# Performance work log

Measured on AMD Instinct MI355X. Metric: run time of the kernel, lower is better.

## Reference

```python
import jax, jax.numpy as jnp
import numpy as np

NEG = -1e10
EPS = 1e-5
H = 4  # num_heads


def layer_norm(y, g, b):
    m = jnp.mean(y, axis=-1, keepdims=True)
    v = jnp.mean((y - m) ** 2, axis=-1, keepdims=True)
    return (y - m) * jax.lax.rsqrt(v + EPS) * g + b


def setup_inputs() -> dict:
    key = jax.random.key(0)
    B, N, C = 16, 1024, 256
    ks = jax.random.split(key, 12)
    std = 0.1  # matches trunc_normal_(std=0.1) init
    inp = {
        "x": jax.random.normal(ks[0], (B, N, C), jnp.float32),
        "K": jax.random.normal(ks[1], (B, N, N), jnp.float32),
        "n1": jax.random.randint(ks[2], (B,), 8, 33),
        "n2": jax.random.randint(ks[3], (B,), 8, 33),
        "qkv_w": jax.random.normal(ks[4], (3 * C, C), jnp.float32) * std,
        "qkv_b": jnp.zeros((3 * C,), jnp.float32),
        "proj_w": jax.random.normal(ks[5], (C, C), jnp.float32) * std,
        "proj_b": jnp.zeros((C,), jnp.float32),
        "ln1_g": jnp.ones((C,), jnp.float32),
        "ln1_b": jnp.zeros((C,), jnp.float32),
        "ln2_g": jnp.ones((C,), jnp.float32),
        "ln2_b": jnp.zeros((C,), jnp.float32),
        "fc1_w": jax.random.normal(ks[6], (4 * C, C), jnp.float32) * std,
        "fc1_b": jnp.zeros((4 * C,), jnp.float32),
        "fc2_w": jax.random.normal(ks[7], (C, 4 * C), jnp.float32) * std,
        "fc2_b": jnp.zeros((C,), jnp.float32),
    }
    return inp


def reference(x, K, n1, n2, qkv_w, qkv_b, proj_w, proj_b,
              ln1_g, ln1_b, ln2_g, ln2_b, fc1_w, fc1_b, fc2_w, fc2_b):
    B, N, C = x.shape
    D = C // H
    scale = D ** -0.5

    # --- attention block ---
    h = layer_norm(x, ln1_g, ln1_b)
    qkv = (h @ qkv_w.T + qkv_b).reshape(B, N, 3, H, D)
    qkv = jnp.transpose(qkv, (2, 0, 3, 1, 4))  # [3,B,H,N,D]
    q, k, v = qkv[0], qkv[1], qkv[2]

    attn = jnp.einsum('bhnd,bhmd->bhnm', q, k) * scale  # [B,H,N,N]

    # per-sample dynamic block mask: rows>=n1*n2 fully masked; cols>=n1*n2 masked
    nrc = (n1 * n2)[:, None]                  # [B,1]
    invalid = jnp.arange(N)[None, :] >= nrc   # [B,N]
    mask = invalid[:, :, None] | invalid[:, None, :]  # [B,N,N]
    attn = jnp.where(mask[:, None], NEG, attn)
    attn = attn + K[:, None]                  # broadcast K over heads

    a = jax.nn.softmax(attn, axis=-1)
    o = jnp.einsum('bhnm,bhmd->bhnd', a, v)
    o = jnp.transpose(o, (0, 2, 1, 3)).reshape(B, N, C)
    x = x + (o @ proj_w.T + proj_b)

    # --- MLP block (exact GELU as torch nn.GELU) ---
    h2 = layer_norm(x, ln2_g, ln2_b)
    m = jax.nn.gelu(h2 @ fc1_w.T + fc1_b, approximate=False)
    m = m @ fc2_w.T + fc2_b
    return x + m
```

## Files before the change

kernel.cpp:

```cpp
#include <hip/hip_runtime.h>
#include <math.h>
#include <stdint.h>

constexpr int Bc = 16, Nn = 1024, Cc = 256, Hh = 4;
constexpr int Mrows = Bc * Nn;
constexpr float EPSV = 1e-5f;

typedef __attribute__((ext_vector_type(4))) float f32x4;
typedef __attribute__((ext_vector_type(8))) short bf16x8;

__device__ inline float wave_reduce_sum(float v) {
#pragma unroll
  for (int m = 32; m >= 1; m >>= 1) v += __shfl_xor(v, m);
  return v;
}

__device__ inline short f2bf(float f) {
  uint32_t u = __builtin_bit_cast(uint32_t, f);
  u = (u + 0x7fffu + ((u >> 16) & 1u)) >> 16;
  return (short)u;
}
__device__ inline float bf2f(short s) {
  uint32_t u = ((uint32_t)(uint16_t)s) << 16;
  return __builtin_bit_cast(float, u);
}

__device__ inline float gelu_fast(float x) {
  float x2 = x * x;
  float u = x * (0.7978845608028654f + 0.0356774081f * x2);
  float e = __builtin_amdgcn_exp2f(u * 2.8853900817779268f);
  return x * (1.f - __builtin_amdgcn_rcpf(e + 1.f));
}

#define GLDS(gptr, lptr)                                             \
  __builtin_amdgcn_global_load_lds(                                  \
      (const __attribute__((address_space(1))) void*)(gptr),         \
      (__attribute__((address_space(3))) void*)(lptr), 16, 0, 0)

__global__ __launch_bounds__(256)
void cvt_all(const float* __restrict__ s0, short* __restrict__ d0,
             const float* __restrict__ s1, short* __restrict__ d1,
             const float* __restrict__ s2, short* __restrict__ d2,
             const float* __restrict__ s3, short* __restrict__ d3) {
  int bid = blockIdx.x;
  const float* s;
  short* d;
  int base;
  if (bid < 192)      { s = s0; d = d0; base = bid; }
  else if (bid < 256) { s = s1; d = d1; base = bid - 192; }
  else if (bid < 512) { s = s2; d = d2; base = bid - 256; }
  else                { s = s3; d = d3; base = bid - 512; }
  int i = (base * 256 + threadIdx.x) * 4;
  float4 v = *(const float4*)(s + i);
  short4 o;
  o.x = f2bf(v.x); o.y = f2bf(v.y); o.z = f2bf(v.z); o.w = f2bf(v.w);
  *(short4*)(d + i) = o;
}

__global__ __launch_bounds__(256)
void ln_kernel(const float* __restrict__ x, const float* __restrict__ g,
               const float* __restrict__ b, short* __restrict__ h) {
  int row = blockIdx.x * 4 + (threadIdx.x >> 6);
  int lane = threadIdx.x & 63;
  const float4* xr = (const float4*)(x + (size_t)row * Cc);
  float4 v = xr[lane];
  float s = v.x + v.y + v.z + v.w;
  float sq = v.x * v.x + v.y * v.y + v.z * v.z + v.w * v.w;
  s = wave_reduce_sum(s);
  sq = wave_reduce_sum(sq);
  float mean = s * (1.f / Cc);
  float var = sq * (1.f / Cc) - mean * mean;
  float inv = rsqrtf(var + EPSV);
  float4 gg = ((const float4*)g)[lane];
  float4 bb = ((const float4*)b)[lane];
  short4 o;
  o.x = f2bf((v.x - mean) * inv * gg.x + bb.x);
  o.y = f2bf((v.y - mean) * inv * gg.y + bb.y);
  o.z = f2bf((v.z - mean) * inv * gg.z + bb.z);
  o.w = f2bf((v.w - mean) * inv * gg.w + bb.w);
  *(short4*)(h + (size_t)row * Cc + lane * 4) = o;
}

__global__ __launch_bounds__(256)
void qkv_mfma(const short* __restrict__ A, const short* __restrict__ Bw,
              const float* __restrict__ bias, short* __restrict__ qkp,
              short* __restrict__ vtp) {
  __shared__ __align__(16) short As[128 * 64];
  __shared__ __align__(16) short Bs[128 * 64];
  int t = threadIdx.x;
  int w = t >> 6, lane = t & 63;
  int wm = w >> 1, wn = w & 1;
  int l16 = lane & 15, lhi = lane >> 4;
  int m0 = blockIdx.y * 128, n0 = blockIdx.x * 128;
  const bool vblk = (n0 >= 512);
  f32x4 acc[4][4] = {};

  for (int k0 = 0; k0 < 256; k0 += 64) {
    __syncthreads();
#pragma unroll
    for (int i = 0; i < 4; ++i) {
      int cc = i * 256 + t;
      int r = cc >> 3, sl = cc & 7, ssl = sl ^ (r & 7);
      GLDS(A + (size_t)(m0 + r) * 256 + k0 + ssl * 8, &As[cc * 8]);
      GLDS(Bw + (size_t)(n0 + r) * 256 + k0 + ssl * 8, &Bs[cc * 8]);
    }
    asm volatile("s_waitcnt vmcnt(0)" ::: "memory");
    __syncthreads();
    if (!vblk) {
#pragma unroll
      for (int ks = 0; ks < 2; ++ks) {
        bf16x8 af[4], bg[4];
#pragma unroll
        for (int mi = 0; mi < 4; ++mi) {
          int row = wm * 64 + mi * 16 + l16;
          af[mi] = *(const bf16x8*)&As[row * 64 + ((ks * 32 + lhi * 8) ^ ((row & 7) << 3))];
        }
#pragma unroll
        for (int ni = 0; ni < 4; ++ni) {
          int row = wn * 64 + ni * 16 + l16;
          bg[ni] = *(const bf16x8*)&Bs[row * 64 + ((ks * 32 + lhi * 8) ^ ((row & 7) << 3))];
        }
#pragma unroll
        for (int mi = 0; mi < 4; ++mi)
#pragma unroll
          for (int ni = 0; ni < 4; ++ni)
            acc[mi][ni] = __builtin_amdgcn_mfma_f32_16x16x32_bf16(
                af[mi], bg[ni], acc[mi][ni], 0, 0, 0);
      }
    } else {
#pragma unroll
      for (int ks = 0; ks < 2; ++ks) {
        bf16x8 af[4], bg[4];
#pragma unroll
        for (int mi = 0; mi < 4; ++mi) {
          int row = wm * 64 + mi * 16 + l16;
          af[mi] = *(const bf16x8*)&As[row * 64 + ((ks * 32 + lhi * 8) ^ ((row & 7) << 3))];
        }
#pragma unroll
        for (int ni = 0; ni < 4; ++ni) {
          int row = wn * 64 + ni * 16 + l16;
          bg[ni] = *(const bf16x8*)&Bs[row * 64 + ((ks * 32 + lhi * 8) ^ ((row & 7) << 3))];
        }
#pragma unroll
        for (int mi = 0; mi < 4; ++mi)
#pragma unroll
          for (int ni = 0; ni < 4; ++ni)
            acc[mi][ni] = __builtin_amdgcn_mfma_f32_16x16x32_bf16(
                bg[ni], af[mi], acc[mi][ni], 0, 0, 0);
      }
    }
  }

  if (!vblk) {
    const bool isq = (n0 < 256);
#pragma unroll
    for (int mi = 0; mi < 4; ++mi) {
      int mbase = m0 + wm * 64 + mi * 16 + lhi * 4;
#pragma unroll
      for (int ni = 0; ni < 4; ++ni) {
        int n = n0 + wn * 64 + ni * 16 + l16;
        int s = n >> 8, hh = (n >> 6) & 3, d = n & 63;
        float bv = bias[n];
#pragma unroll
        for (int r = 0; r < 4; ++r) {
          int m = mbase + r;
          int b = m >> 10, rw = m & 1023;
          float v = acc[mi][ni][r] + bv;
          if (isq) v *= 0.125f;
          qkp[(size_t)s * 4194304 + (((size_t)(b * 4 + hh)) * 1024 + rw) * 64 + d] = f2bf(v);
        }
      }
    }
  } else {
#pragma unroll
    for (int mi = 0; mi < 4; ++mi) {
#pragma unroll
      for (int ni = 0; ni < 4; ++ni) {
#pragma unroll
        for (int r = 0; r < 4; ++r) {
          int n = n0 + wn * 64 + ni * 16 + lhi * 4 + r;
          int hh = (n >> 6) & 3, d = n & 63;
          int m = m0 + wm * 64 + mi * 16 + l16;
          int b = m >> 10, rw = m & 1023;
          float v = acc[mi][ni][r] + bias[n];
          vtp[(((size_t)(b * 4 + hh)) * 64 + d) * 1024 + rw] = f2bf(v);
        }
      }
    }
  }
}

__global__ __launch_bounds__(256)
void vmean_kernel(const short* __restrict__ vt, short* __restrict__ vmb) {
  __shared__ float part[64][4];
  int bh = blockIdx.x;
  int d = threadIdx.x >> 2, seg = threadIdx.x & 3;
  const short* p = vt + (size_t)bh * 65536 + (size_t)d * 1024 + seg * 256;
  float s = 0.f;
  for (int i = 0; i < 256; i += 8) {
    bf16x8 v = *(const bf16x8*)(p + i);
#pragma unroll
    for (int j = 0; j < 8; ++j) s += bf2f(v[j]);
  }
  part[d][seg] = s;
  __syncthreads();
  if (threadIdx.x < 64) {
    int dd = threadIdx.x;
    float tot = part[dd][0] + part[dd][1] + part[dd][2] + part[dd][3];
    vmb[bh * 64 + dd] = f2bf(tot * (1.f / 1024.f));
  }
}

__global__ __launch_bounds__(256)
void fattn_mfma(const short* __restrict__ qpk, const short* __restrict__ kpk,
                const short* __restrict__ vt, const float* __restrict__ Kmat,
                const int* __restrict__ n1, const int* __restrict__ n2,
                const short* __restrict__ vmb, short* __restrict__ o,
                float* __restrict__ pO, float* __restrict__ pL, int zsplit) {
  int bh = blockIdx.y, b = bh >> 2, hh = bh & 3;
  int qt = blockIdx.x;
  int row0 = qt * 64;
  int sp = blockIdx.z;
  int t = threadIdx.x;
  int w = t >> 6, lane = t & 63, l16 = lane & 15, lhi = lane >> 4;

  const short* qb = qpk + (size_t)bh * 65536 + (size_t)(row0 + w * 16 + l16) * 64;
  bf16x8 qf0 = *(const bf16x8*)(qb + lhi * 8);
  bf16x8 qf1 = *(const bf16x8*)(qb + 32 + lhi * 8);

  int nc = n1[b] * n2[b];
  __shared__ short vms[64];
  if (t < 64) vms[t] = vmb[bh * 64 + t];
  __syncthreads();
  if (row0 >= nc) {
    if (sp == 0) {
      for (int idx = t; idx < 4096; idx += 256) {
        int r = idx >> 6, d = idx & 63;
        o[((size_t)(b * 1024 + row0 + r)) * 256 + hh * 64 + d] = vms[d];
      }
    }
    return;
  }
  int ntiles = (nc + 63) >> 6;
  int TPS = (zsplit == 1) ? ntiles : ((ntiles + 3) >> 2);
  int nsp = (ntiles + TPS - 1) / TPS;
  int jt0 = sp * TPS;
  if (jt0 >= ntiles) return;
  int jstart = jt0 * 64;
  int jend = min(jstart + TPS * 64, nc);
  const bool final_out = (nsp == 1);

  __shared__ __align__(16) short Ks[2][64 * 64];
  __shared__ __align__(16) short Vs[2][64 * 64];
  __shared__ __align__(16) short Ps[64 * 64];

  constexpr float LOG2E = 1.4426950408889634f;
  constexpr float MREF = 12.0f;

  f32x4 accO[4] = {};
  float lsum[4] = {};
  const float* Kb = Kmat + (size_t)b * 1048576 + (size_t)(row0 + w * 16) * 1024;

  f32x4 kvp[4];

#pragma unroll
  for (int i = 0; i < 2; ++i) {
    int cc = i * 256 + t;
    int r = cc >> 3, sl = cc & 7, ssl = sl ^ (r & 7);
    GLDS(kpk + (size_t)bh * 65536 + (size_t)(jstart + r) * 64 + ssl * 8, &Ks[0][cc * 8]);
    GLDS(vt + (size_t)bh * 65536 + (size_t)r * 1024 + jstart + ssl * 8, &Vs[0][cc * 8]);
  }
#pragma unroll
  for (int ni = 0; ni < 4; ++ni)
#pragma unroll
    for (int r = 0; r < 4; ++r)
      kvp[ni][r] =
          (Kb[(size_t)(lhi * 4 + r) * 1024 + jstart + ni * 16 + l16] - MREF) * LOG2E;

  int cur = 0;
  for (int j0 = jstart; j0 < jend; j0 += 64, cur ^= 1) {
    asm volatile("s_waitcnt vmcnt(0)" ::: "memory");
    __syncthreads();

    f32x4 kvc[4];
#pragma unroll
    for (int i = 0; i < 4; ++i) kvc[i] = kvp[i];
    int jn = j0 + 64;
    if (jn < jend) {
      int nxt = cur ^ 1;
#pragma unroll
      for (int i = 0; i < 2; ++i) {
        int cc = i * 256 + t;
        int r = cc >> 3, sl = cc & 7, ssl = sl ^ (r & 7);
        GLDS(kpk + (size_t)bh * 65536 + (size_t)(jn + r) * 64 + ssl * 8, &Ks[nxt][cc * 8]);
        GLDS(vt + (size_t)bh * 65536 + (size_t)r * 1024 + jn + ssl * 8, &Vs[nxt][cc * 8]);
      }
#pragma unroll
      for (int ni = 0; ni < 4; ++ni)
#pragma unroll
        for (int r = 0; r < 4; ++r)
          kvp[ni][r] =
              (Kb[(size_t)(lhi * 4 + r) * 1024 + jn + ni * 16 + l16] - MREF) * LOG2E;
    }

    f32x4 accS[4] = {};
#pragma unroll
    for (int ks = 0; ks < 2; ++ks) {
#pragma unroll
      for (int ni = 0; ni < 4; ++ni) {
        int row = ni * 16 + l16;
        bf16x8 kf = *(const bf16x8*)&Ks[cur][row * 64 + (((ks * 4 + lhi) ^ (row & 7)) << 3)];
        accS[ni] = __builtin_amdgcn_mfma_f32_16x16x32_bf16(
            ks ? qf1 : qf0, kf, accS[ni], 0, 0, 0);
      }
    }

#pragma unroll
    for (int ni = 0; ni < 4; ++ni) {
      bool valid = (j0 + ni * 16 + l16) < nc;
#pragma unroll
      for (int r = 0; r < 4; ++r) {
        float e = __builtin_amdgcn_exp2f(fmaf(accS[ni][r], LOG2E, kvc[ni][r]));
        e = valid ? e : 0.f;
        lsum[r] += e;
        int prow = w * 16 + lhi * 4 + r;
        int col = ni * 16 + l16;
        Ps[prow * 64 + ((((col >> 3) ^ (prow & 7)) << 3) | (col & 7))] = f2bf(e);
      }
    }

#pragma unroll
    for (int ks = 0; ks < 2; ++ks) {
      int prow = w * 16 + l16;
      bf16x8 pf = *(const bf16x8*)&Ps[prow * 64 + (((ks * 4 + lhi) ^ (prow & 7)) << 3)];
#pragma unroll
      for (int ni = 0; ni < 4; ++ni) {
        int vrow = ni * 16 + l16;
        bf16x8 vf = *(const bf16x8*)&Vs[cur][vrow * 64 + (((ks * 4 + lhi) ^ (vrow & 7)) << 3)];
        accO[ni] = __builtin_amdgcn_mfma_f32_16x16x32_bf16(pf, vf, accO[ni], 0, 0, 0);
      }
    }
  }

#pragma unroll
  for (int r = 0; r < 4; ++r) {
    lsum[r] += __shfl_xor(lsum[r], 1);
    lsum[r] += __shfl_xor(lsum[r], 2);
    lsum[r] += __shfl_xor(lsum[r], 4);
    lsum[r] += __shfl_xor(lsum[r], 8);
  }

  if (final_out) {
#pragma unroll
    for (int ni = 0; ni < 4; ++ni) {
#pragma unroll
      for (int r = 0; r < 4; ++r) {
        int row = row0 + w * 16 + lhi * 4 + r;
        int d = ni * 16 + l16;
        short ov;
        if (row < nc) ov = f2bf(accO[ni][r] * (1.f / lsum[r]));
        else ov = vms[d];
        o[((size_t)(b * 1024 + row)) * 256 + hh * 64 + d] = ov;
      }
    }
  } else {
    float* po = pO + (((size_t)sp * 64 + bh) * 16 + qt) * 4096;
#pragma unroll
    for (int ni = 0; ni < 4; ++ni)
#pragma unroll
      for (int r = 0; r < 4; ++r)
        po[(w * 16 + lhi * 4 + r) * 64 + ni * 16 + l16] = accO[ni][r];
    if (l16 == 0) {
      float* pl = pL + (((size_t)sp * 64 + bh) * 16 + qt) * 64;
#pragma unroll
      for (int r = 0; r < 4; ++r) pl[w * 16 + lhi * 4 + r] = lsum[r];
    }
    if (sp == 0) {
      for (int idx = t; idx < 4096; idx += 256) {
        int r = idx >> 6, d = idx & 63;
        int row = row0 + r;
        if (row >= nc)
          o[((size_t)(b * 1024 + row)) * 256 + hh * 64 + d] = vms[d];
      }
    }
  }
}

__global__ __launch_bounds__(256)
void fattn_combine(const float* __restrict__ pO, const float* __restrict__ pL,
                   const int* __restrict__ n1, const int* __restrict__ n2,
                   short* __restrict__ o) {
  int bh = blockIdx.y, b = bh >> 2, hh = bh & 3;
  int qt = blockIdx.x;
  int row0 = qt * 64;
  int nc = n1[b] * n2[b];
  if (row0 >= nc) return;
  int ntiles = (nc + 63) >> 6;
  int TPS = (ntiles + 3) >> 2;
  int nsp = (ntiles + TPS - 1) / TPS;
  if (nsp < 2) return;

  int t = threadIdx.x;
  int q = t >> 2, ds = (t & 3) * 16;
  int row = row0 + q;
  if (row >= nc) return;

  const size_t spstrideO = (size_t)64 * 16 * 4096;
  const size_t spstrideL = (size_t)64 * 16 * 64;
  const float* baseO = pO + ((size_t)bh * 16 + qt) * 4096 + q * 64 + ds;
  const float* baseL = pL + ((size_t)bh * 16 + qt) * 64 + q;

  f32x4 s[4] = {};
  float L = 0.f;
  for (int sp = 0; sp < nsp; ++sp) {
    const float* p = baseO + sp * spstrideO;
#pragma unroll
    for (int i = 0; i < 4; ++i) s[i] += *(const f32x4*)(p + i * 4);
    L += baseL[sp * spstrideL];
  }
  float rl = 1.f / L;
  short* op = o + ((size_t)(b * 1024 + row)) * 256 + hh * 64 + ds;
#pragma unroll
  for (int i = 0; i < 4; ++i) {
    short4 ov;
    ov.x = f2bf(s[i][0] * rl);
    ov.y = f2bf(s[i][1] * rl);
    ov.z = f2bf(s[i][2] * rl);
    ov.w = f2bf(s[i][3] * rl);
    *(short4*)(op + i * 4) = ov;
  }
}

template <bool GELU, bool RES, bool OUTF, bool OUTB>
__global__ __launch_bounds__(256)
void gemm_mfma(const short* __restrict__ A, const short* __restrict__ Bw,
               const float* __restrict__ bias, const float* __restrict__ resid,
               float* __restrict__ Cf, short* __restrict__ Cb,
               int M, int Nd, int Kd) {
  __shared__ __align__(16) short As[128 * 64];
  __shared__ __align__(16) short Bs[128 * 64];
  int t = threadIdx.x;
  int w = t >> 6, lane = t & 63;
  int wm = w >> 1, wn = w & 1;
  int l16 = lane & 15, lhi = lane >> 4;
  int m0 = blockIdx.y * 128, n0 = blockIdx.x * 128;
  f32x4 acc[4][4] = {};

  for (int k0 = 0; k0 < Kd; k0 += 64) {
    __syncthreads();
#pragma unroll
    for (int i = 0; i < 4; ++i) {
      int cc = i * 256 + t;
      int r = cc >> 3, sl = cc & 7, ssl = sl ^ (r & 7);
      GLDS(A + (size_t)(m0 + r) * Kd + k0 + ssl * 8, &As[cc * 8]);
      GLDS(Bw + (size_t)(n0 + r) * Kd + k0 + ssl * 8, &Bs[cc * 8]);
    }
    asm volatile("s_waitcnt vmcnt(0)" ::: "memory");
    __syncthreads();
#pragma unroll
    for (int ks = 0; ks < 2; ++ks) {
      bf16x8 af[4], bg[4];
#pragma unroll
      for (int mi = 0; mi < 4; ++mi) {
        int row = wm * 64 + mi * 16 + l16;
        af[mi] = *(const bf16x8*)&As[row * 64 + ((ks * 32 + lhi * 8) ^ ((row & 7) << 3))];
      }
#pragma unroll
      for (int ni = 0; ni < 4; ++ni) {
        int row = wn * 64 + ni * 16 + l16;
        bg[ni] = *(const bf16x8*)&Bs[row * 64 + ((ks * 32 + lhi * 8) ^ ((row & 7) << 3))];
      }
#pragma unroll
      for (int mi = 0; mi < 4; ++mi)
#pragma unroll
        for (int ni = 0; ni < 4; ++ni)
          acc[mi][ni] = __builtin_amdgcn_mfma_f32_16x16x32_bf16(
              af[mi], bg[ni], acc[mi][ni], 0, 0, 0);
    }
  }
#pragma unroll
  for (int mi = 0; mi < 4; ++mi) {
    int rbase = m0 + wm * 64 + mi * 16 + lhi * 4;
#pragma unroll
    for (int ni = 0; ni < 4; ++ni) {
      int n = n0 + wn * 64 + ni * 16 + l16;
      float bv = bias[n];
#pragma unroll
      for (int r = 0; r < 4; ++r) {
        int m = rbase + r;
        float v = acc[mi][ni][r] + bv;
        if (GELU) v = gelu_fast(v);
        size_t idx = (size_t)m * Nd + n;
        if (RES) v += resid[idx];
        if (OUTF) Cf[idx] = v;
        if (OUTB) Cb[idx] = f2bf(v);
      }
    }
  }
}

template <bool GELU, bool RES, bool OUTF, bool OUTB>
__global__ __launch_bounds__(256)
void gemm64_mfma(const short* __restrict__ A, const short* __restrict__ Bw,
                 const float* __restrict__ bias, const float* __restrict__ resid,
                 float* __restrict__ Cf, short* __restrict__ Cb,
                 int M, int Nd, int Kd) {
  __shared__ __align__(16) short As[64 * 64];
  __shared__ __align__(16) short Bs[128 * 64];
  int t = threadIdx.x;
  int w = t >> 6, lane = t & 63;
  int l16 = lane & 15, lhi = lane >> 4;
  int m0 = blockIdx.y * 64, n0 = blockIdx.x * 128;
  f32x4 acc[4][2] = {};

  for (int k0 = 0; k0 < Kd; k0 += 64) {
    __syncthreads();
#pragma unroll
    for (int i = 0; i < 2; ++i) {
      int cc = i * 256 + t;
      int r = cc >> 3, sl = cc & 7, ssl = sl ^ (r & 7);
      GLDS(A + (size_t)(m0 + r) * Kd + k0 + ssl * 8, &As[cc * 8]);
    }
#pragma unroll
    for (int i = 0; i < 4; ++i) {
      int cc = i * 256 + t;
      int r = cc >> 3, sl = cc & 7, ssl = sl ^ (r & 7);
      GLDS(Bw + (size_t)(n0 + r) * Kd + k0 + ssl * 8, &Bs[cc * 8]);
    }
    asm volatile("s_waitcnt vmcnt(0)" ::: "memory");
    __syncthreads();
#pragma unroll
    for (int ks = 0; ks < 2; ++ks) {
      bf16x8 af[4], bg[2];
#pragma unroll
      for (int mi = 0; mi < 4; ++mi) {
        int row = mi * 16 + l16;
        af[mi] = *(const bf16x8*)&As[row * 64 + ((ks * 32 + lhi * 8) ^ ((row & 7) << 3))];
      }
#pragma unroll
      for (int ni = 0; ni < 2; ++ni) {
        int row = w * 32 + ni * 16 + l16;
        bg[ni] = *(const bf16x8*)&Bs[row * 64 + ((ks * 32 + lhi * 8) ^ ((row & 7) << 3))];
      }
#pragma unroll
      for (int mi = 0; mi < 4; ++mi)
#pragma unroll
        for (int ni = 0; ni < 2; ++ni)
          acc[mi][ni] = __builtin_amdgcn_mfma_f32_16x16x32_bf16(
              af[mi], bg[ni], acc[mi][ni], 0, 0, 0);
    }
  }
#pragma unroll
  for (int mi = 0; mi < 4; ++mi) {
    int rbase = m0 + mi * 16 + lhi * 4;
#pragma unroll
    for (int ni = 0; ni < 2; ++ni) {
      int n = n0 + w * 32 + ni * 16 + l16;
      float bv = bias[n];
#pragma unroll
      for (int r = 0; r < 4; ++r) {
        int m = rbase + r;
        float v = acc[mi][ni][r] + bv;
        if (GELU) v = gelu_fast(v);
        size_t idx = (size_t)m * Nd + n;
        if (RES) v += resid[idx];
        if (OUTF) Cf[idx] = v;
        if (OUTB) Cb[idx] = f2bf(v);
      }
    }
  }
}

extern "C" void kernel_launch(void* const* d_in, const int* in_sizes, int n_in,
                              void* d_out, int out_size, void* d_ws, size_t ws_size,
                              hipStream_t stream) {
  const float* x      = (const float*)d_in[0];
  const float* Kmat   = (const float*)d_in[1];
  const int*   n1     = (const int*)d_in[2];
  const int*   n2     = (const int*)d_in[3];
  const float* qkv_w  = (const float*)d_in[4];
  const float* qkv_b  = (const float*)d_in[5];
  const float* proj_w = (const float*)d_in[6];
  const float* proj_b = (const float*)d_in[7];
  const float* ln1_g  = (const float*)d_in[8];
  const float* ln1_b  = (const float*)d_in[9];
  const float* ln2_g  = (const float*)d_in[10];
  const float* ln2_b  = (const float*)d_in[11];
  const float* fc1_w  = (const float*)d_in[12];
  const float* fc1_b  = (const float*)d_in[13];
  const float* fc2_w  = (const float*)d_in[14];
  const float* fc2_b  = (const float*)d_in[15];
  float* out = (float*)d_out;

  char* ws = (char*)d_ws;
  constexpr size_t MB = 1024 * 1024;
  short* hb    = (short*)ws;
  short* qkp   = (short*)(ws + 8 * MB);
  short* vtp   = (short*)(ws + 24 * MB);
  short* m1    = (short*)(ws + 8 * MB);
  short* vmb   = (short*)(ws + 40 * MB);
  short* wqkv  = (short*)(ws + 41 * MB);
  short* wproj = (short*)(ws + 42 * MB);
  short* wfc1  = (short*)(ws + 43 * MB);
  short* wfc2  = (short*)(ws + 44 * MB);
  float* pO    = (float*)(ws + 48 * MB);
  float* pL    = (float*)(ws + 116 * MB);
  short* obuf  = hb;
  short* qpk   = qkp;
  short* kpk   = qkp + 4194304;

  const bool split = ws_size >= (size_t)118 * MB;

  cvt_all<<<dim3(768), 256, 0, stream>>>(qkv_w, wqkv, proj_w, wproj,
                                         fc1_w, wfc1, fc2_w, wfc2);
  ln_kernel<<<dim3(Mrows / 4), 256, 0, stream>>>(x, ln1_g, ln1_b, hb);
  qkv_mfma<<<dim3(6, 128), 256, 0, stream>>>(hb, wqkv, qkv_b, qkp, vtp);
  vmean_kernel<<<dim3(Bc * Hh), 256, 0, stream>>>(vtp, vmb);
  if (split) {
    fattn_mfma<<<dim3(Nn / 64, Bc * Hh, 4), 256, 0, stream>>>(
        qpk, kpk, vtp, Kmat, n1, n2, vmb, obuf, pO, pL, 4);
    fattn_combine<<<dim3(Nn / 64, Bc * Hh), 256, 0, stream>>>(
        pO, pL, n1, n2, obuf);
  } else {
    fattn_mfma<<<dim3(Nn / 64, Bc * Hh, 1), 256, 0, stream>>>(
        qpk, kpk, vtp, Kmat, n1, n2, vmb, obuf, pO, pL, 1);
  }
  gemm64_mfma<false, true, true, false><<<dim3(2, 256), 256, 0, stream>>>(
      obuf, wproj, proj_b, x, out, nullptr, Mrows, 256, 256);
  ln_kernel<<<dim3(Mrows / 4), 256, 0, stream>>>(out, ln2_g, ln2_b, hb);
  gemm_mfma<true, false, false, true><<<dim3(8, 128), 256, 0, stream>>>(
      hb, wfc1, fc1_b, nullptr, nullptr, m1, Mrows, 1024, 256);
  gemm64_mfma<false, true, true, false><<<dim3(2, 256), 256, 0, stream>>>(
      m1, wfc2, fc2_b, out, out, nullptr, Mrows, 256, 1024);
}
```

Before: 141.9 us.

## Replace attention grid with persistent work-queue kernel sorted by sequence length

Builds a per-call work queue of (batch, head, query-tile, split) items ordered by descending valid length. A fixed set of persistent blocks then pulls items atomically instead of launching a full grid where many blocks exit early. The masked-row mean fill moves into a separate small kernel. This aims to cut wasted block launches and tail imbalance across batches, at the cost of two extra launches, a serial single-thread queue build and a per-item atomic.

```diff
diff --git a/kernel.cpp b/kernel.cpp
--- a/kernel.cpp
+++ b/kernel.cpp
@@ -212,175 +212,228 @@
 }
 
 __global__ __launch_bounds__(256)
-void fattn_mfma(const short* __restrict__ qpk, const short* __restrict__ kpk,
+void build_queue(const int* __restrict__ n1, const int* __restrict__ n2,
+                 int* __restrict__ q) {
+  __shared__ int ncs[16], order[16], boff[17];
+  int t = threadIdx.x;
+  if (t < 16) ncs[t] = n1[t] * n2[t];
+  __syncthreads();
+  if (t == 0) {
+    for (int i = 0; i < 16; ++i) order[i] = i;
+    for (int i = 1; i < 16; ++i) {
+      int oi = order[i], key = ncs[oi], j = i - 1;
+      while (j >= 0 && ncs[order[j]] < key) { order[j + 1] = order[j]; --j; }
+      order[j + 1] = oi;
+    }
+    int off = 0;
+    for (int i = 0; i < 16; ++i) {
+      boff[i] = off;
+      int nc = ncs[order[i]];
+      int nt = (nc + 63) >> 6;
+      int tps = (nt + 3) >> 2;
+      int nsp = (nt + tps - 1) / tps;
+      off += 4 * nt * nsp;
+    }
+    boff[16] = off;
+    q[0] = 0;
+    q[1] = off;
+  }
+  __syncthreads();
+  int M = boff[16];
+  for (int idx = t; idx < M; idx += 256) {
+    int s = 0;
+    while (boff[s + 1] <= idx) ++s;
+    int loc = idx - boff[s];
+    int b = order[s];
+    int nc = ncs[b];
+    int nt = (nc + 63) >> 6;
+    int tps = (nt + 3) >> 2;
+    int nsp = (nt + tps - 1) / tps;
+    int sp = loc % nsp;
+    int hq = loc / nsp;
+    int qt = hq % nt;
+    int h = hq / nt;
+    q[2 + idx] = ((b * 4 + h) << 6) | (qt << 2) | sp;
+  }
+}
+
+__global__ __launch_bounds__(256)
+void fill_mean(const int* __restrict__ n1, const int* __restrict__ n2,
+               const short* __restrict__ vmb, short* __restrict__ o) {
+  int bh = blockIdx.x, b = bh >> 2, hh = bh & 3;
+  int nc = n1[b] * n2[b];
+  int row0 = ((nc + 63) >> 6) * 64;
+  int t = threadIdx.x;
+  short vm = vmb[bh * 64 + (t & 63)];
+  for (int r = row0 + (t >> 6); r < 1024; r += 4)
+    o[((size_t)(b * 1024 + r)) * 256 + hh * 64 + (t & 63)] = vm;
+}
+
+__global__ __launch_bounds__(256)
+void fattn_pers(const short* __restrict__ qpk, const short* __restrict__ kpk,
                 const short* __restrict__ vt, const float* __restrict__ Kmat,
                 const int* __restrict__ n1, const int* __restrict__ n2,
                 const short* __restrict__ vmb, short* __restrict__ o,
-                float* __restrict__ pO, float* __restrict__ pL, int zsplit) {
-  int bh = blockIdx.y, b = bh >> 2, hh = bh & 3;
-  int qt = blockIdx.x;
-  int row0 = qt * 64;
-  int sp = blockIdx.z;
-  int t = threadIdx.x;
-  int w = t >> 6, lane = t & 63, l16 = lane & 15, lhi = lane >> 4;
-
-  const short* qb = qpk + (size_t)bh * 65536 + (size_t)(row0 + w * 16 + l16) * 64;
-  bf16x8 qf0 = *(const bf16x8*)(qb + lhi * 8);
-  bf16x8 qf1 = *(const bf16x8*)(qb + 32 + lhi * 8);
-
-  int nc = n1[b] * n2[b];
-  __shared__ short vms[64];
-  if (t < 64) vms[t] = vmb[bh * 64 + t];
-  __syncthreads();
-  if (row0 >= nc) {
-    if (sp == 0) {
-      for (int idx = t; idx < 4096; idx += 256) {
-        int r = idx >> 6, d = idx & 63;
-        o[((size_t)(b * 1024 + row0 + r)) * 256 + hh * 64 + d] = vms[d];
-      }
-    }
-    return;
-  }
-  int ntiles = (nc + 63) >> 6;
-  int TPS = (zsplit == 1) ? ntiles : ((ntiles + 3) >> 2);
-  int nsp = (ntiles + TPS - 1) / TPS;
-  int jt0 = sp * TPS;
-  if (jt0 >= ntiles) return;
-  int jstart = jt0 * 64;
-  int jend = min(jstart + TPS * 64, nc);
-  const bool final_out = (nsp == 1);
-
+                float* __restrict__ pO, float* __restrict__ pL,
+                int* __restrict__ q) {
+  __shared__ int sitem;
   __shared__ __align__(16) short Ks[2][64 * 64];
   __shared__ __align__(16) short Vs[2][64 * 64];
   __shared__ __align__(16) short Ps[64 * 64];
+  int t = threadIdx.x;
+  int w = t >> 6, lane = t & 63, l16 = lane & 15, lhi = lane >> 4;
+  const int M = q[1];
 
   constexpr float LOG2E = 1.4426950408889634f;
   constexpr float MREF = 12.0f;
 
-  f32x4 accO[4] = {};
-  float lsum[4] = {};
-  const float* Kb = Kmat + (size_t)b * 1048576 + (size_t)(row0 + w * 16) * 1024;
-
-  f32x4 kvp[4];
-
-#pragma unroll
-  for (int i = 0; i < 2; ++i) {
-    int cc = i * 256 + t;
-    int r = cc >> 3, sl = cc & 7, ssl = sl ^ (r & 7);
-    GLDS(kpk + (size_t)bh * 65536 + (size_t)(jstart + r) * 64 + ssl * 8, &Ks[0][cc * 8]);
-    GLDS(vt + (size_t)bh * 65536 + (size_t)r * 1024 + jstart + ssl * 8, &Vs[0][cc * 8]);
-  }
-#pragma unroll
-  for (int ni = 0; ni < 4; ++ni)
-#pragma unroll
-    for (int r = 0; r < 4; ++r)
-      kvp[ni][r] =
-          (Kb[(size_t)(lhi * 4 + r) * 1024 + jstart + ni * 16 + l16] - MREF) * LOG2E;
-
-  int cur = 0;
-  for (int j0 = jstart; j0 < jend; j0 += 64, cur ^= 1) {
-    asm volatile("s_waitcnt vmcnt(0)" ::: "memory");
-    __syncthreads();
-
-    f32x4 kvc[4];
-#pragma unroll
-    for (int i = 0; i < 4; ++i) kvc[i] = kvp[i];
-    int jn = j0 + 64;
-    if (jn < jend) {
-      int nxt = cur ^ 1;
-#pragma unroll
-      for (int i = 0; i < 2; ++i) {
-        int cc = i * 256 + t;
-        int r = cc >> 3, sl = cc & 7, ssl = sl ^ (r & 7);
-        GLDS(kpk + (size_t)bh * 65536 + (size_t)(jn + r) * 64 + ssl * 8, &Ks[nxt][cc * 8]);
-        GLDS(vt + (size_t)bh * 65536 + (size_t)r * 1024 + jn + ssl * 8, &Vs[nxt][cc * 8]);
-      }
+  while (true) {
+    __syncthreads();
+    if (t == 0) sitem = atomicAdd(q, 1);
+    __syncthreads();
+    int ii = sitem;
+    if (ii >= M) break;
+    int item = q[2 + ii];
+    int sp = item & 3, qt = (item >> 2) & 15, bh = item >> 6;
+    int b = bh >> 2, hh = bh & 3;
+    int row0 = qt * 64;
+    int nc = n1[b] * n2[b];
+    int ntiles = (nc + 63) >> 6;
+    int TPS = (ntiles + 3) >> 2;
+    int nsp = (ntiles + TPS - 1) / TPS;
+    int jstart = sp * TPS * 64;
+    int jend = min(jstart + TPS * 64, nc);
+    const bool final_out = (nsp == 1);
+
+    const short* qb = qpk + (size_t)bh * 65536 + (size_t)(row0 + w * 16 + l16) * 64;
+    bf16x8 qf0 = *(const bf16x8*)(qb + lhi * 8);
+    bf16x8 qf1 = *(const bf16x8*)(qb + 32 + lhi * 8);
+
+    f32x4 accO[4] = {};
+    float lsum[4] = {};
+    const float* Kb = Kmat + (size_t)b * 1048576 + (size_t)(row0 + w * 16) * 1024;
+
+    f32x4 kvp[4];
+
+#pragma unroll
+    for (int i = 0; i < 2; ++i) {
+      int cc = i * 256 + t;
+      int r = cc >> 3, sl = cc & 7, ssl = sl ^ (r & 7);
+      GLDS(kpk + (size_t)bh * 65536 + (size_t)(jstart + r) * 64 + ssl * 8, &Ks[0][cc * 8]);
+      GLDS(vt + (size_t)bh * 65536 + (size_t)r * 1024 + jstart + ssl * 8, &Vs[0][cc * 8]);
+    }
+#pragma unroll
+    for (int ni = 0; ni < 4; ++ni)
+#pragma unroll
+      for (int r = 0; r < 4; ++r)
+        kvp[ni][r] =
+            (Kb[(size_t)(lhi * 4 + r) * 1024 + jstart + ni * 16 + l16] - MREF) * LOG2E;
+
+    int cur = 0;
+    for (int j0 = jstart; j0 < jend; j0 += 64, cur ^= 1) {
+      asm volatile("s_waitcnt vmcnt(0)" ::: "memory");
+      __syncthreads();
+
+      f32x4 kvc[4];
+#pragma unroll
+      for (int i = 0; i < 4; ++i) kvc[i] = kvp[i];
+      int jn = j0 + 64;
+      if (jn < jend) {
+        int nxt = cur ^ 1;
+#pragma unroll
+        for (int i = 0; i < 2; ++i) {
+          int cc = i * 256 + t;
+          int r = cc >> 3, sl = cc & 7, ssl = sl ^ (r & 7);
+          GLDS(kpk + (size_t)bh * 65536 + (size_t)(jn + r) * 64 + ssl * 8, &Ks[nxt][cc * 8]);
+          GLDS(vt + (size_t)bh * 65536 + (size_t)r * 1024 + jn + ssl * 8, &Vs[nxt][cc * 8]);
+        }
+#pragma unroll
+        for (int ni = 0; ni < 4; ++ni)
+#pragma unroll
+          for (int r = 0; r < 4; ++r)
+            kvp[ni][r] =
+                (Kb[(size_t)(lhi * 4 + r) * 1024 + jn + ni * 16 + l16] - MREF) * LOG2E;
+      }
+
+      f32x4 accS[4] = {};
+#pragma unroll
+      for (int ks = 0; ks < 2; ++ks) {
+#pragma unroll
+        for (int ni = 0; ni < 4; ++ni) {
+          int row = ni * 16 + l16;
+          bf16x8 kf = *(const bf16x8*)&Ks[cur][row * 64 + (((ks * 4 + lhi) ^ (row & 7)) << 3)];
+          accS[ni] = __builtin_amdgcn_mfma_f32_16x16x32_bf16(
+              ks ? qf1 : qf0, kf, accS[ni], 0, 0, 0);
+        }
+      }
+
+#pragma unroll
+      for (int ni = 0; ni < 4; ++ni) {
+        bool valid = (j0 + ni * 16 + l16) < nc;
+#pragma unroll
+        for (int r = 0; r < 4; ++r) {
+          float e = __builtin_amdgcn_exp2f(fmaf(accS[ni][r], LOG2E, kvc[ni][r]));
+          e = valid ? e : 0.f;
+          lsum[r] += e;
+          int prow = w * 16 + lhi * 4 + r;
+          int col = ni * 16 + l16;
+          Ps[prow * 64 + ((((col >> 3) ^ (prow & 7)) << 3) | (col & 7))] = f2bf(e);
+        }
+      }
+
+#pragma unroll
+      for (int ks = 0; ks < 2; ++ks) {
+        int prow = w * 16 + l16;
+        bf16x8 pf = *(const bf16x8*)&Ps[prow * 64 + (((ks * 4 + lhi) ^ (prow & 7)) << 3)];
+#pragma unroll
+        for (int ni = 0; ni < 4; ++ni) {
+          int vrow = ni * 16 + l16;
+          bf16x8 vf = *(const bf16x8*)&Vs[cur][vrow * 64 + (((ks * 4 + lhi) ^ (vrow & 7)) << 3)];
+          accO[ni] = __builtin_amdgcn_mfma_f32_16x16x32_bf16(pf, vf, accO[ni], 0, 0, 0);
+        }
+      }
+    }
+
+#pragma unroll
+    for (int r = 0; r < 4; ++r) {
+      lsum[r] += __shfl_xor(lsum[r], 1);
+      lsum[r] += __shfl_xor(lsum[r], 2);
+      lsum[r] += __shfl_xor(lsum[r], 4);
+      lsum[r] += __shfl_xor(lsum[r], 8);
+    }
+
+    if (final_out) {
+#pragma unroll
+      for (int ni = 0; ni < 4; ++ni) {
+#pragma unroll
+        for (int r = 0; r < 4; ++r) {
+          int row = row0 + w * 16 + lhi * 4 + r;
+          int d = ni * 16 + l16;
+          short ov;
+          if (row < nc) ov = f2bf(accO[ni][r] * (1.f / lsum[r]));
+          else ov = vmb[bh * 64 + d];
+          o[((size_t)(b * 1024 + row)) * 256 + hh * 64 + d] = ov;
+        }
+      }
+    } else {
+      float* po = pO + (((size_t)sp * 64 + bh) * 16 + qt) * 4096;
 #pragma unroll
       for (int ni = 0; ni < 4; ++ni)
 #pragma unroll
         for (int r = 0; r < 4; ++r)
-          kvp[ni][r] =
-              (Kb[(size_t)(lhi * 4 + r) * 1024 + jn + ni * 16 + l16] - MREF) * LOG2E;
-    }
-
-    f32x4 accS[4] = {};
-#pragma unroll
-    for (int ks = 0; ks < 2; ++ks) {
-#pragma unroll
-      for (int ni = 0; ni < 4; ++ni) {
-        int row = ni * 16 + l16;
-        bf16x8 kf = *(const bf16x8*)&Ks[cur][row * 64 + (((ks * 4 + lhi) ^ (row & 7)) << 3)];
-        accS[ni] = __builtin_amdgcn_mfma_f32_16x16x32_bf16(
-            ks ? qf1 : qf0, kf, accS[ni], 0, 0, 0);
-      }
-    }
-
-#pragma unroll
-    for (int ni = 0; ni < 4; ++ni) {
-      bool valid = (j0 + ni * 16 + l16) < nc;
-#pragma unroll
-      for (int r = 0; r < 4; ++r) {
-        float e = __builtin_amdgcn_exp2f(fmaf(accS[ni][r], LOG2E, kvc[ni][r]));
-        e = valid ? e : 0.f;
-        lsum[r] += e;
-        int prow = w * 16 + lhi * 4 + r;
-        int col = ni * 16 + l16;
-        Ps[prow * 64 + ((((col >> 3) ^ (prow & 7)) << 3) | (col & 7))] = f2bf(e);
-      }
-    }
-
-#pragma unroll
-    for (int ks = 0; ks < 2; ++ks) {
-      int prow = w * 16 + l16;
-      bf16x8 pf = *(const bf16x8*)&Ps[prow * 64 + (((ks * 4 + lhi) ^ (prow & 7)) << 3)];
-#pragma unroll
-      for (int ni = 0; ni < 4; ++ni) {
-        int vrow = ni * 16 + l16;
-        bf16x8 vf = *(const bf16x8*)&Vs[cur][vrow * 64 + (((ks * 4 + lhi) ^ (vrow & 7)) << 3)];
-        accO[ni] = __builtin_amdgcn_mfma_f32_16x16x32_bf16(pf, vf, accO[ni], 0, 0, 0);
-      }
-    }
-  }
-
-#pragma unroll
-  for (int r = 0; r < 4; ++r) {
-    lsum[r] += __shfl_xor(lsum[r], 1);
-    lsum[r] += __shfl_xor(lsum[r], 2);
-    lsum[r] += __shfl_xor(lsum[r], 4);
-    lsum[r] += __shfl_xor(lsum[r], 8);
-  }
-
-  if (final_out) {
-#pragma unroll
-    for (int ni = 0; ni < 4; ++ni) {
-#pragma unroll
-      for (int r = 0; r < 4; ++r) {
-        int row = row0 + w * 16 + lhi * 4 + r;
-        int d = ni * 16 + l16;
-        short ov;
-        if (row < nc) ov = f2bf(accO[ni][r] * (1.f / lsum[r]));
-        else ov = vms[d];
-        o[((size_t)(b * 1024 + row)) * 256 + hh * 64 + d] = ov;
-      }
-    }
-  } else {
-    float* po = pO + (((size_t)sp * 64 + bh) * 16 + qt) * 4096;
-#pragma unroll
-    for (int ni = 0; ni < 4; ++ni)
-#pragma unroll
-      for (int r = 0; r < 4; ++r)
-        po[(w * 16 + lhi * 4 + r) * 64 + ni * 16 + l16] = accO[ni][r];
-    if (l16 == 0) {
-      float* pl = pL + (((size_t)sp * 64 + bh) * 16 + qt) * 64;
-#pragma unroll
-      for (int r = 0; r < 4; ++r) pl[w * 16 + lhi * 4 + r] = lsum[r];
-    }
-    if (sp == 0) {
-      for (int idx = t; idx < 4096; idx += 256) {
-        int r = idx >> 6, d = idx & 63;
-        int row = row0 + r;
-        if (row >= nc)
-          o[((size_t)(b * 1024 + row)) * 256 + hh * 64 + d] = vms[d];
+          po[(w * 16 + lhi * 4 + r) * 64 + ni * 16 + l16] = accO[ni][r];
+      if (l16 == 0) {
+        float* pl = pL + (((size_t)sp * 64 + bh) * 16 + qt) * 64;
+#pragma unroll
+        for (int r = 0; r < 4; ++r) pl[w * 16 + lhi * 4 + r] = lsum[r];
+      }
+      if (sp == 0) {
+        for (int idx = t; idx < 4096; idx += 256) {
+          int r = idx >> 6, d = idx & 63;
+          int row = row0 + r;
+          if (row >= nc)
+            o[((size_t)(b * 1024 + row)) * 256 + hh * 64 + d] = vmb[bh * 64 + d];
+        }
       }
     }
   }
@@ -605,6 +658,7 @@
   short* wfc2  = (short*)(ws + 44 * MB);
   float* pO    = (float*)(ws + 48 * MB);
   float* pL    = (float*)(ws + 116 * MB);
+  int*   qq    = (int*)(ws + 117 * MB);
   short* obuf  = hb;
   short* qpk   = qkp;
   short* kpk   = qkp + 4194304;
@@ -617,13 +671,20 @@
   qkv_mfma<<<dim3(6, 128), 256, 0, stream>>>(hb, wqkv, qkv_b, qkp, vtp);
   vmean_kernel<<<dim3(Bc * Hh), 256, 0, stream>>>(vtp, vmb);
   if (split) {
-    fattn_mfma<<<dim3(Nn / 64, Bc * Hh, 4), 256, 0, stream>>>(
-        qpk, kpk, vtp, Kmat, n1, n2, vmb, obuf, pO, pL, 4);
+    build_queue<<<dim3(1), 256, 0, stream>>>(n1, n2, qq);
+    fill_mean<<<dim3(Bc * Hh), 256, 0, stream>>>(n1, n2, vmb, obuf);
+    fattn_pers<<<dim3(768), 256, 0, stream>>>(
+        qpk, kpk, vtp, Kmat, n1, n2, vmb, obuf, pO, pL, qq);
     fattn_combine<<<dim3(Nn / 64, Bc * Hh), 256, 0, stream>>>(
         pO, pL, n1, n2, obuf);
   } else {
-    fattn_mfma<<<dim3(Nn / 64, Bc * Hh, 1), 256, 0, stream>>>(
-        qpk, kpk, vtp, Kmat, n1, n2, vmb, obuf, pO, pL, 1);
+    int* qq2 = (int*)(ws + 45 * MB);
+    build_queue<<<dim3(1), 256, 0, stream>>>(n1, n2, qq2);
+    fill_mean<<<dim3(Bc * Hh), 256, 0, stream>>>(n1, n2, vmb, obuf);
+    fattn_pers<<<dim3(768), 256, 0, stream>>>(
+        qpk, kpk, vtp, Kmat, n1, n2, vmb, obuf, pO, pL, qq2);
+    fattn_combine<<<dim3(Nn / 64, Bc * Hh), 256, 0, stream>>>(
+        pO, pL, n1, n2, obuf);
   }
   gemm64_mfma<false, true, true, false><<<dim3(2, 256), 256, 0, stream>>>(
       obuf, wproj, proj_b, x, out, nullptr, Mrows, 256, 256);
```

After: 166.3 us. +17.2%, slower.
